# Optimization experiments

Hardware: AMD Instinct MI355X
Metric: run time of the kernel (lower is better)

## Reference

```python
import jax, jax.numpy as jnp
import numpy as np

B, C, IN = 8, 1024, 256
OUT, H, NS, SD = 256, 4, 5, 64
DK = OUT // H


def setup_inputs() -> dict:
    key = jax.random.key(0)
    ks = jax.random.split(key, 16)
    s = lambda k, *shape: jax.random.normal(k, shape, dtype=jnp.float32) * 0.05
    return {
        "x": jax.random.normal(ks[0], (B, C, IN), dtype=jnp.float32),
        "A_prior": jax.random.uniform(ks[1], (C, C), dtype=jnp.float32),
        # lin_project
        "Wp": s(ks[2], IN, OUT), "bp": jnp.zeros((OUT,), jnp.float32),
        # stage_mlp: Linear(IN,128) -> ReLU -> Linear(128,NS)
        "Ws1": s(ks[3], IN, 128), "bs1": jnp.zeros((128,), jnp.float32),
        "Ws2": s(ks[4], 128, NS), "bs2": jnp.zeros((NS,), jnp.float32),
        # mlp_c: Linear(NS,SD) -> ReLU -> Linear(SD,SD)
        "Wc1": s(ks[5], NS, SD), "bc1": jnp.zeros((SD,), jnp.float32),
        "Wc2": s(ks[6], SD, SD), "bc2": jnp.zeros((SD,), jnp.float32),
        # att_scorer: Linear(2*DK+SD, 1, bias=False) -> weight vector
        "att_w": s(ks[7], 2 * DK + SD),
        "lam": jnp.ones((H,), jnp.float32),
    }


def reference(x, A_prior, Wp, bp, Ws1, bs1, Ws2, bs2, Wc1, bc1, Wc2, bc2, att_w, lam):
    # projection -> (B, C, H, DK)
    x_proj = (x @ Wp + bp).reshape(B, C, H, DK)
    # stage logits from mean-pooled features
    s_logits = jax.nn.relu(x.mean(axis=1) @ Ws1 + bs1) @ Ws2 + bs2  # (B, NS)
    s_prob = jax.nn.softmax(s_logits, axis=-1)
    c = jax.nn.relu(s_prob @ Wc1 + bc1) @ Wc2 + bc2  # (B, SD)
    # att_scorer is linear over cat([x_src, x_dst, c]); decompose weight to
    # avoid materializing the (B,C,C,H,2*DK+SD) concat tensor.
    w_src, w_dst, w_c = att_w[:DK], att_w[DK:2 * DK], att_w[2 * DK:]
    src_s = jnp.einsum('bjhd,d->bjh', x_proj, w_src)  # x_src[b,i,j] = x_proj[b,j]
    dst_s = jnp.einsum('bihd,d->bih', x_proj, w_dst)  # x_dst[b,i,j] = x_proj[b,i]
    c_s = c @ w_c                                      # (B,)
    e = jax.nn.leaky_relu(
        src_s[:, None, :, :] + dst_s[:, :, None, :] + c_s[:, None, None, None],
        negative_slope=0.2)                            # (B, C, C, H)
    prior = lam[None, None, None, :] * jnp.log(A_prior[None, :, :, None] + 1e-9)
    alpha = jax.nn.softmax(e + prior, axis=2)          # softmax over src j
    out = jnp.einsum('bijh,bjhd->bihd', alpha, x_proj).reshape(B, C, OUT)
    return out, s_logits
```

## Files before the change

### kernel.cpp

```cpp
#include <hip/hip_runtime.h>
#include <hip/hip_fp16.h>

typedef _Float16 f16x8 __attribute__((ext_vector_type(8)));
typedef _Float16 f16x4 __attribute__((ext_vector_type(4)));
typedef float f32x4 __attribute__((ext_vector_type(4)));

#define NB 8
#define NNS 5


__global__ __launch_bounds__(256) void k_pre(const float* __restrict__ Wp,
                                             const float* __restrict__ x,
                                             const float* __restrict__ A,
                                             __half* __restrict__ WpF,
                                             float* __restrict__ xmean,
                                             __half* __restrict__ xF,
                                             __half* __restrict__ l2AF) {
  __shared__ __align__(16) float xs[32][260];
  const int t = threadIdx.x;
  const int blk = blockIdx.x;
  if (blk < 256) {
    const int idx = (blk << 8) + t;
    const int u = idx & 7, lane = (idx >> 3) & 63;
    const int kc = (idx >> 9) & 7, nt = (idx >> 12) & 3, nh = idx >> 14;
    const int f = (nh << 6) + (nt << 4) + (lane & 15);
    const int k = (kc << 5) + ((lane >> 4) << 3) + u;
    WpF[idx] = __float2half(Wp[(k << 8) + f]);
  } else if (blk < 512) {
    const int row0 = (blk - 256) << 5;
    const int b = row0 >> 10;
    const int rt0 = row0 >> 4;
    float ps = 0.f;
    #pragma unroll 8
    for (int r = 0; r < 32; ++r) {
      const float v = x[(size_t)(row0 + r) * 256 + t];
      xs[r][t] = v;
      ps += v;
    }
    atomicAdd(&xmean[(b << 8) + t], ps);
    __syncthreads();
    #pragma unroll
    for (int it = 0; it < 4; ++it) {
      const int oi = it * 256 + t;
      const int lane = oi & 63;
      const int kc = (oi >> 6) & 7;
      const int rtl = oi >> 9;
      const int row_l = (rtl << 4) + (lane & 15);
      const int k0 = (kc << 5) + ((lane >> 4) << 3);
      const f32x4 va = *(const f32x4*)&xs[row_l][k0];
      const f32x4 vb = *(const f32x4*)&xs[row_l][k0 + 4];
      f16x8 hv;
      #pragma unroll
      for (int u = 0; u < 4; ++u) {
        hv[u] = (_Float16)va[u];
        hv[u + 4] = (_Float16)vb[u];
      }
      *(f16x8*)(xF + (((size_t)(rt0 + rtl)) << 12) + (kc << 9) + (lane << 3)) =
          hv;
    }
  } else {
    const int idx = ((blk - 512) << 8) + t;
    const int u = idx & 7, lane = (idx >> 3) & 63;
    const int jc = (idx >> 9) & 31, it = idx >> 14;
    const int row = (it << 4) + (lane & 15);
    const int j = (jc << 5) + ((lane >> 4) << 3) + u;
    l2AF[idx] = __float2half(__log2f(A[((size_t)row << 10) + j] + 1e-9f));
  }
}

__global__ __launch_bounds__(256, 4) void k_projM(
    const __half* __restrict__ xF, const __half* __restrict__ WpF,
    const float* __restrict__ bp, const float* __restrict__ att_w,
    __half* __restrict__ xpF, float* __restrict__ srcT,
    float* __restrict__ dstT) {
  const int t = threadIdx.x;
  const int l = t & 63, w = t >> 6;
  const int lm = l & 15, q = l >> 4;
  const int rg = blockIdx.x >> 2, nh = blockIdx.x & 3;
  const int rt = (rg << 2) + w;
  const int R0 = rt << 4;

  const __half* Ap = xF + (((size_t)rt) << 12) + (l << 3);
  const __half* Bw = WpF + (nh << 14) + (l << 3);

  f16x8 ah[8];
  #pragma unroll
  for (int kc = 0; kc < 8; ++kc) ah[kc] = *(const f16x8*)(Ap + (kc << 9));

  f32x4 acc0 = {0.f, 0.f, 0.f, 0.f}, acc1 = acc0, acc2 = acc0, acc3 = acc0;
  #pragma unroll
  for (int kc = 0; kc < 8; ++kc) {
    const f16x8 b0 = *(const f16x8*)(Bw + (kc << 9));
    const f16x8 b1 = *(const f16x8*)(Bw + (kc << 9) + 4096);
    const f16x8 b2 = *(const f16x8*)(Bw + (kc << 9) + 8192);
    const f16x8 b3 = *(const f16x8*)(Bw + (kc << 9) + 12288);
    acc0 = __builtin_amdgcn_mfma_f32_16x16x32_f16(ah[kc], b0, acc0, 0, 0, 0);
    acc1 = __builtin_amdgcn_mfma_f32_16x16x32_f16(ah[kc], b1, acc1, 0, 0, 0);
    acc2 = __builtin_amdgcn_mfma_f32_16x16x32_f16(ah[kc], b2, acc2, 0, 0, 0);
    acc3 = __builtin_amdgcn_mfma_f32_16x16x32_f16(ah[kc], b3, acc3, 0, 0, 0);
  }

  const int b = R0 >> 10;
  const int il = (R0 & 1023) + (q << 2);
  const int jc = il >> 5, lq = (il >> 3) & 3, u0 = il & 7;
  const int lane_o = (lq << 4) + lm;
  f32x4 accs[4] = {acc0, acc1, acc2, acc3};
  float wsn[4], wdn[4];
  #pragma unroll
  for (int n = 0; n < 4; ++n) {
    const int d = (n << 4) + lm;
    wsn[n] = att_w[d];
    wdn[n] = att_w[64 + d];
  }
  const size_t base = ((((size_t)((b << 2) + nh) << 5) + jc) << 2);
  #pragma unroll
  for (int n = 0; n < 4; ++n) {
    const float bias = bp[(nh << 6) + (n << 4) + lm];
    f16x4 o;
    #pragma unroll
    for (int reg = 0; reg < 4; ++reg) {
      accs[n][reg] += bias;
      o[reg] = (_Float16)accs[n][reg];
    }
    *(f16x4*)(xpF + (((base + n) << 9) + (lane_o << 3) + u0)) = o;
  }
  #pragma unroll
  for (int reg = 0; reg < 4; ++reg) {
    float ss = 0.f, ds = 0.f;
    #pragma unroll
    for (int n = 0; n < 4; ++n) {
      ss = fmaf(accs[n][reg], wsn[n], ss);
      ds = fmaf(accs[n][reg], wdn[n], ds);
    }
    #pragma unroll
    for (int off = 1; off < 16; off <<= 1) {
      ss += __shfl_xor(ss, off);
      ds += __shfl_xor(ds, off);
    }
    if (lm == 0) {
      const int i = il + reg;
      srcT[(((b << 2) + nh) << 10) + i] = ss;
      dstT[(((b << 2) + nh) << 10) + i] = ds;
    }
  }
}

__global__ __launch_bounds__(256) void k_head(
    const float* __restrict__ Ws1, const float* __restrict__ bs1,
    const float* __restrict__ Ws2, const float* __restrict__ bs2,
    const float* __restrict__ Wc1, const float* __restrict__ bc1,
    const float* __restrict__ Wc2, const float* __restrict__ bc2,
    const float* __restrict__ att_w, const float* __restrict__ xmean,
    float* __restrict__ cs_ws, float* __restrict__ out_slogits) {
  __shared__ float xm[256];
  __shared__ float h1p[2][128];
  __shared__ float h1[128];
  __shared__ float sl[NNS];
  __shared__ float sp[NNS];
  __shared__ float cc1[64];
  __shared__ float cvec[64];
  const int b = blockIdx.x, t = threadIdx.x;
  xm[t] = xmean[b * 256 + t] * (1.f / 1024.f);
  __syncthreads();
  {
    const int kh = t >> 7, f = t & 127;
    const float* wcol = Ws1 + (kh << 7) * 128 + f;
    const float* xk = xm + (kh << 7);
    float a = 0.f;
    #pragma unroll 8
    for (int k = 0; k < 128; ++k) a = fmaf(xk[k], wcol[k * 128], a);
    h1p[kh][f] = a;
  }
  __syncthreads();
  if (t < 128) h1[t] = fmaxf(h1p[0][t] + h1p[1][t] + bs1[t], 0.f);
  __syncthreads();
  if (t < NNS) {
    float a = bs2[t];
    #pragma unroll 8
    for (int k = 0; k < 128; ++k) a = fmaf(h1[k], Ws2[k * NNS + t], a);
    sl[t] = a;
    out_slogits[b * NNS + t] = a;
  }
  __syncthreads();
  if (t == 0) {
    float m = sl[0];
    for (int n = 1; n < NNS; ++n) m = fmaxf(m, sl[n]);
    float s = 0.f;
    for (int n = 0; n < NNS; ++n) { sp[n] = expf(sl[n] - m); s += sp[n]; }
    for (int n = 0; n < NNS; ++n) sp[n] /= s;
  }
  __syncthreads();
  if (t < 64) {
    float a = bc1[t];
    #pragma unroll
    for (int n = 0; n < NNS; ++n) a = fmaf(sp[n], Wc1[n * 64 + t], a);
    cc1[t] = fmaxf(a, 0.f);
  }
  __syncthreads();
  if (t < 64) {
    float a = bc2[t];
    #pragma unroll 8
    for (int m = 0; m < 64; ++m) a = fmaf(cc1[m], Wc2[m * 64 + t], a);
    cvec[t] = a;
  }
  __syncthreads();
  if (t < 64) {
    float v = cvec[t] * att_w[128 + t];
    #pragma unroll
    for (int m = 32; m; m >>= 1) v += __shfl_xor(v, m);
    if (t == 0) cs_ws[b] = v;
  }
}

__global__ __launch_bounds__(512, 4) void k_attn(
    const __half* __restrict__ xpF, const __half* __restrict__ l2AF,
    const float* __restrict__ srcT, const float* __restrict__ dstT,
    const float* __restrict__ cs_ws, const float* __restrict__ lam,
    float* __restrict__ out) {
  __shared__ float red[4][4][16][18];
  __shared__ float dsum[4][2][16];
  const int t = threadIdx.x;
  const int l = t & 63, w = t >> 6;
  const int h = w & 3, jh = w >> 2;
  const int lm = l & 15, q = l >> 4;
  const int b = blockIdx.x >> 6;
  const int tile = blockIdx.x & 63;
  const int i0 = tile << 4;

  const float csv = cs_ws[b];
  const float lamln2 = lam[h] * 0.69314718056f;
  const float dstc = dstT[(((b << 2) + h) << 10) + i0 + lm] + csv;

  const __half* Lp = l2AF + (tile << 14) + (jh << 13) + (l << 3);
  const float* Sp = srcT + (((b << 2) + h) << 10) + (jh << 9) + (q << 3);
  const __half* Bp =
      xpF + (((size_t)((b << 2) + h)) << 16) + (jh << 15) + (l << 3);

  f32x4 acc0 = {0.f, 0.f, 0.f, 0.f}, acc1 = acc0, acc2 = acc0, acc3 = acc0;
  float sum = 0.f;

  f16x8 la = *(const f16x8*)Lp;
  f32x4 s0 = *(const f32x4*)Sp;
  f32x4 s1 = *(const f32x4*)(Sp + 4);
  f16x8 bf0 = *(const f16x8*)Bp;
  f16x8 bf1 = *(const f16x8*)(Bp + 512);
  f16x8 bf2 = *(const f16x8*)(Bp + 1024);
  f16x8 bf3 = *(const f16x8*)(Bp + 1536);

  #pragma unroll 4
  for (int kk = 0; kk < 16; ++kk) {
    const int nk = (kk < 15) ? kk + 1 : kk;
    const f16x8 la_n = *(const f16x8*)(Lp + (nk << 9));
    const f32x4 s0_n = *(const f32x4*)(Sp + (nk << 5));
    const f32x4 s1_n = *(const f32x4*)(Sp + (nk << 5) + 4);
    const f16x8 b0_n = *(const f16x8*)(Bp + (nk << 11));
    const f16x8 b1_n = *(const f16x8*)(Bp + (nk << 11) + 512);
    const f16x8 b2_n = *(const f16x8*)(Bp + (nk << 11) + 1024);
    const f16x8 b3_n = *(const f16x8*)(Bp + (nk << 11) + 1536);

    f16x8 af;
    #pragma unroll
    for (int u = 0; u < 4; ++u) {
      float e0 = s0[u] + dstc;
      e0 = fmaxf(e0, 0.2f * e0);
      const float p0 = __expf(fmaf(lamln2, (float)la[u], e0));
      sum += p0;
      af[u] = (_Float16)p0;
      float e1 = s1[u] + dstc;
      e1 = fmaxf(e1, 0.2f * e1);
      const float p1 = __expf(fmaf(lamln2, (float)la[u + 4], e1));
      sum += p1;
      af[u + 4] = (_Float16)p1;
    }
    acc0 = __builtin_amdgcn_mfma_f32_16x16x32_f16(af, bf0, acc0, 0, 0, 0);
    acc1 = __builtin_amdgcn_mfma_f32_16x16x32_f16(af, bf1, acc1, 0, 0, 0);
    acc2 = __builtin_amdgcn_mfma_f32_16x16x32_f16(af, bf2, acc2, 0, 0, 0);
    acc3 = __builtin_amdgcn_mfma_f32_16x16x32_f16(af, bf3, acc3, 0, 0, 0);
    la = la_n; s0 = s0_n; s1 = s1_n;
    bf0 = b0_n; bf1 = b1_n; bf2 = b2_n; bf3 = b3_n;
  }

  sum += __shfl_xor(sum, 16);
  sum += __shfl_xor(sum, 32);
  if (l < 16) dsum[h][jh][lm] = sum;
  if (jh == 1) {
    #pragma unroll
    for (int reg = 0; reg < 4; ++reg) {
      const int mrow = (q << 2) + reg;
      red[h][0][mrow][lm] = acc0[reg];
      red[h][1][mrow][lm] = acc1[reg];
      red[h][2][mrow][lm] = acc2[reg];
      red[h][3][mrow][lm] = acc3[reg];
    }
  }
  __syncthreads();
  if (jh == 0) {
    float* ob = out + (((size_t)((b << 10) + i0)) << 8) + (h << 6) + lm;
    #pragma unroll
    for (int reg = 0; reg < 4; ++reg) {
      const int mrow = (q << 2) + reg;
      const float dv = 1.f / (dsum[h][0][mrow] + dsum[h][1][mrow]);
      float* orow = ob + ((size_t)mrow << 8);
      orow[0] = (acc0[reg] + red[h][0][mrow][lm]) * dv;
      orow[16] = (acc1[reg] + red[h][1][mrow][lm]) * dv;
      orow[32] = (acc2[reg] + red[h][2][mrow][lm]) * dv;
      orow[48] = (acc3[reg] + red[h][3][mrow][lm]) * dv;
    }
  }
}

extern "C" void kernel_launch(void* const* d_in, const int* in_sizes, int n_in,
                              void* d_out, int out_size, void* d_ws,
                              size_t ws_size, hipStream_t stream) {
  const float* x     = (const float*)d_in[0];
  const float* A     = (const float*)d_in[1];
  const float* Wp    = (const float*)d_in[2];
  const float* bp    = (const float*)d_in[3];
  const float* Ws1   = (const float*)d_in[4];
  const float* bs1   = (const float*)d_in[5];
  const float* Ws2   = (const float*)d_in[6];
  const float* bs2   = (const float*)d_in[7];
  const float* Wc1   = (const float*)d_in[8];
  const float* bc1   = (const float*)d_in[9];
  const float* Wc2   = (const float*)d_in[10];
  const float* bc2   = (const float*)d_in[11];
  const float* att_w = (const float*)d_in[12];
  const float* lam   = (const float*)d_in[13];
  float* out = (float*)d_out;
  float* ws  = (float*)d_ws;

  __half* xpF  = (__half*)ws;
  __half* l2AF = (__half*)(ws + 1048576);
  __half* xF   = (__half*)(ws + 1572864);
  float* srcT  = ws + 2621440;
  float* dstT  = ws + 2654208;
  float* xmean = ws + 2686976;
  float* cs    = ws + 2689024;
  __half* WpF  = (__half*)(ws + 2689032);

  hipMemsetAsync(xmean, 0, 2048 * sizeof(float), stream);

  k_pre<<<dim3(4608), dim3(256), 0, stream>>>(Wp, x, A, WpF, xmean, xF, l2AF);
  k_projM<<<dim3(512), dim3(256), 0, stream>>>(xF, WpF, bp, att_w, xpF, srcT,
                                               dstT);
  k_head<<<dim3(NB), dim3(256), 0, stream>>>(Ws1, bs1, Ws2, bs2, Wc1, bc1,
                                             Wc2, bc2, att_w, xmean, cs,
                                             out + NB * 1024 * 256);
  k_attn<<<dim3(512), dim3(512), 0, stream>>>(xpF, l2AF, srcT, dstT, cs, lam,
                                              out);
}
```

Baseline: 129.0 us.

## Replace atomic mean with partial sums and double attention row tile per block

The mean-pool no longer uses atomicAdd into a zeroed buffer, which needed a separate memset. Each row block now writes a partial sum, and k_head adds up the 32 partials per batch. k_attn now runs 1024-thread blocks covering 32 query rows (two 16-row subtiles), halving the grid so that the srcT and xpF B-fragment loads can be shared through cache across subtiles. The larger blocks may reduce occupancy flexibility, and __launch_bounds__(1024,4) may force register pressure.

```diff
diff --git a/kernel.cpp b/kernel.cpp
--- a/kernel.cpp
+++ b/kernel.cpp
@@ -13,7 +13,7 @@
                                              const float* __restrict__ x,
                                              const float* __restrict__ A,
                                              __half* __restrict__ WpF,
-                                             float* __restrict__ xmean,
+                                             float* __restrict__ xmeanP,
                                              __half* __restrict__ xF,
                                              __half* __restrict__ l2AF) {
   __shared__ __align__(16) float xs[32][260];
@@ -27,8 +27,8 @@
     const int k = (kc << 5) + ((lane >> 4) << 3) + u;
     WpF[idx] = __float2half(Wp[(k << 8) + f]);
   } else if (blk < 512) {
-    const int row0 = (blk - 256) << 5;
-    const int b = row0 >> 10;
+    const int rb = blk - 256;
+    const int row0 = rb << 5;
     const int rt0 = row0 >> 4;
     float ps = 0.f;
     #pragma unroll 8
@@ -37,7 +37,7 @@
       xs[r][t] = v;
       ps += v;
     }
-    atomicAdd(&xmean[(b << 8) + t], ps);
+    xmeanP[(rb << 8) + t] = ps;
     __syncthreads();
     #pragma unroll
     for (int it = 0; it < 4; ++it) {
@@ -150,7 +150,7 @@
     const float* __restrict__ Ws2, const float* __restrict__ bs2,
     const float* __restrict__ Wc1, const float* __restrict__ bc1,
     const float* __restrict__ Wc2, const float* __restrict__ bc2,
-    const float* __restrict__ att_w, const float* __restrict__ xmean,
+    const float* __restrict__ att_w, const float* __restrict__ xmeanP,
     float* __restrict__ cs_ws, float* __restrict__ out_slogits) {
   __shared__ float xm[256];
   __shared__ float h1p[2][128];
@@ -160,7 +160,13 @@
   __shared__ float cc1[64];
   __shared__ float cvec[64];
   const int b = blockIdx.x, t = threadIdx.x;
-  xm[t] = xmean[b * 256 + t] * (1.f / 1024.f);
+  {
+    float s = 0.f;
+    const float* p = xmeanP + (((b << 5)) << 8) + t;
+    #pragma unroll 8
+    for (int g = 0; g < 32; ++g) s += p[g << 8];
+    xm[t] = s * (1.f / 1024.f);
+  }
   __syncthreads();
   {
     const int kh = t >> 7, f = t & 127;
@@ -212,26 +218,27 @@
   }
 }
 
-__global__ __launch_bounds__(512, 4) void k_attn(
+__global__ __launch_bounds__(1024, 4) void k_attn(
     const __half* __restrict__ xpF, const __half* __restrict__ l2AF,
     const float* __restrict__ srcT, const float* __restrict__ dstT,
     const float* __restrict__ cs_ws, const float* __restrict__ lam,
     float* __restrict__ out) {
-  __shared__ float red[4][4][16][18];
-  __shared__ float dsum[4][2][16];
+  __shared__ float red[4][2][4][16][17];
+  __shared__ float dsum[4][2][2][16];
   const int t = threadIdx.x;
   const int l = t & 63, w = t >> 6;
-  const int h = w & 3, jh = w >> 2;
+  const int h = w & 3, jh = (w >> 2) & 1, mt = w >> 3;
   const int lm = l & 15, q = l >> 4;
-  const int b = blockIdx.x >> 6;
-  const int tile = blockIdx.x & 63;
-  const int i0 = tile << 4;
+  const int b = blockIdx.x >> 5;
+  const int tile = blockIdx.x & 31;
+  const int i0 = tile << 5;
+  const int it = (tile << 1) + mt;
 
   const float csv = cs_ws[b];
   const float lamln2 = lam[h] * 0.69314718056f;
-  const float dstc = dstT[(((b << 2) + h) << 10) + i0 + lm] + csv;
-
-  const __half* Lp = l2AF + (tile << 14) + (jh << 13) + (l << 3);
+  const float dstc = dstT[(((b << 2) + h) << 10) + i0 + (mt << 4) + lm] + csv;
+
+  const __half* Lp = l2AF + (((size_t)(it << 5) + (jh << 4)) << 9) + (l << 3);
   const float* Sp = srcT + (((b << 2) + h) << 10) + (jh << 9) + (q << 3);
   const __half* Bp =
       xpF + (((size_t)((b << 2) + h)) << 16) + (jh << 15) + (l << 3);
@@ -282,29 +289,30 @@
 
   sum += __shfl_xor(sum, 16);
   sum += __shfl_xor(sum, 32);
-  if (l < 16) dsum[h][jh][lm] = sum;
+  if (l < 16) dsum[h][jh][mt][lm] = sum;
   if (jh == 1) {
     #pragma unroll
     for (int reg = 0; reg < 4; ++reg) {
       const int mrow = (q << 2) + reg;
-      red[h][0][mrow][lm] = acc0[reg];
-      red[h][1][mrow][lm] = acc1[reg];
-      red[h][2][mrow][lm] = acc2[reg];
-      red[h][3][mrow][lm] = acc3[reg];
+      red[h][mt][0][mrow][lm] = acc0[reg];
+      red[h][mt][1][mrow][lm] = acc1[reg];
+      red[h][mt][2][mrow][lm] = acc2[reg];
+      red[h][mt][3][mrow][lm] = acc3[reg];
     }
   }
   __syncthreads();
   if (jh == 0) {
-    float* ob = out + (((size_t)((b << 10) + i0)) << 8) + (h << 6) + lm;
+    float* ob = out + (((size_t)((b << 10) + i0 + (mt << 4))) << 8) +
+                (h << 6) + lm;
     #pragma unroll
     for (int reg = 0; reg < 4; ++reg) {
       const int mrow = (q << 2) + reg;
-      const float dv = 1.f / (dsum[h][0][mrow] + dsum[h][1][mrow]);
+      const float dv = 1.f / (dsum[h][0][mt][mrow] + dsum[h][1][mt][mrow]);
       float* orow = ob + ((size_t)mrow << 8);
-      orow[0] = (acc0[reg] + red[h][0][mrow][lm]) * dv;
-      orow[16] = (acc1[reg] + red[h][1][mrow][lm]) * dv;
-      orow[32] = (acc2[reg] + red[h][2][mrow][lm]) * dv;
-      orow[48] = (acc3[reg] + red[h][3][mrow][lm]) * dv;
+      orow[0] = (acc0[reg] + red[h][mt][0][mrow][lm]) * dv;
+      orow[16] = (acc1[reg] + red[h][mt][1][mrow][lm]) * dv;
+      orow[32] = (acc2[reg] + red[h][mt][2][mrow][lm]) * dv;
+      orow[48] = (acc3[reg] + red[h][mt][3][mrow][lm]) * dv;
     }
   }
 }
@@ -329,23 +337,21 @@
   float* out = (float*)d_out;
   float* ws  = (float*)d_ws;
 
-  __half* xpF  = (__half*)ws;
-  __half* l2AF = (__half*)(ws + 1048576);
-  __half* xF   = (__half*)(ws + 1572864);
-  float* srcT  = ws + 2621440;
-  float* dstT  = ws + 2654208;
-  float* xmean = ws + 2686976;
-  float* cs    = ws + 2689024;
-  __half* WpF  = (__half*)(ws + 2689032);
-
-  hipMemsetAsync(xmean, 0, 2048 * sizeof(float), stream);
-
-  k_pre<<<dim3(4608), dim3(256), 0, stream>>>(Wp, x, A, WpF, xmean, xF, l2AF);
+  __half* xpF   = (__half*)ws;
+  __half* l2AF  = (__half*)(ws + 1048576);
+  __half* xF    = (__half*)(ws + 1572864);
+  float* srcT   = ws + 2621440;
+  float* dstT   = ws + 2654208;
+  float* xmeanP = ws + 2686976;
+  float* cs     = ws + 2752512;
+  __half* WpF   = (__half*)(ws + 2752520);
+
+  k_pre<<<dim3(4608), dim3(256), 0, stream>>>(Wp, x, A, WpF, xmeanP, xF, l2AF);
   k_projM<<<dim3(512), dim3(256), 0, stream>>>(xF, WpF, bp, att_w, xpF, srcT,
                                                dstT);
   k_head<<<dim3(NB), dim3(256), 0, stream>>>(Ws1, bs1, Ws2, bs2, Wc1, bc1,
-                                             Wc2, bc2, att_w, xmean, cs,
+                                             Wc2, bc2, att_w, xmeanP, cs,
                                              out + NB * 1024 * 256);
-  k_attn<<<dim3(512), dim3(512), 0, stream>>>(xpF, l2AF, srcT, dstT, cs, lam,
-                                              out);
-}
+  k_attn<<<dim3(256), dim3(1024), 0, stream>>>(xpF, l2AF, srcT, dstT, cs, lam,
+                                               out);
+}
```

New measurement: 130.5 us. No clear change (+1.2%).
